# Kernel tuning notes

Measured on AMD Instinct MI355X. Metric: run time of the kernel, lower is better.

The kernel has to match this reference:

```python
import jax, jax.numpy as jnp
import numpy as np

LENS = 4.0
SCALE = 0.25
NUM_HEADS = 16


def _multispike(u):
    # floor(clamp(u, 0, 4) + 0.5)
    return jnp.floor(jnp.clip(u, 0.0, 4.0) + 0.5)


def _ms_act(x):
    # Multispike module: spike(4*x) / 4
    return _multispike(4.0 * x) / 4.0


def setup_inputs() -> dict:
    key = jax.random.key(0)
    ks = jax.random.split(key, 5)
    N, D = 65536, 1024
    x = jax.random.normal(ks[0], (N, D), dtype=jnp.float32)
    s = 1.0 / np.sqrt(D)
    Wq = jax.random.normal(ks[1], (D, D), dtype=jnp.float32) * s
    Wk = jax.random.normal(ks[2], (D, D), dtype=jnp.float32) * s
    Wv = jax.random.normal(ks[3], (D, D), dtype=jnp.float32) * s
    Wp = jax.random.normal(ks[4], (D, D), dtype=jnp.float32) * s
    return {"x": x, "Wq": Wq, "Wk": Wk, "Wv": Wv, "Wp": Wp}


def reference(x, Wq, Wk, Wv, Wp):
    N, C = x.shape
    H = NUM_HEADS
    hd = C // H

    xs = _ms_act(x)
    q = _ms_act(xs @ Wq.T)  # [N, C]
    k = _ms_act(xs @ Wk.T)
    v = _ms_act(xs @ Wv.T)

    q = q.reshape(N, H, hd)
    k = k.reshape(N, H, hd)
    v = v.reshape(N, H, hd)

    # linear attention: kv = k^T @ v per head -> [H, hd, hd]
    kv = jnp.einsum('nhd,nhe->hde', k, v)
    attn = jnp.einsum('nhd,hde->nhe', q, kv) * SCALE  # [N, H, hd]
    attn = attn.reshape(N, C)
    return attn @ Wp.T
```

## Files before the change

kernel.cpp:

```cpp
#include <hip/hip_runtime.h>
#include <hip/hip_bf16.h>


#define N_ROWS 65536
#define DIM    1024

using bf16x8 = __attribute__((ext_vector_type(8))) __bf16;
using f32x4  = __attribute__((ext_vector_type(4))) float;

__device__ __forceinline__ float ms_act(float u) {
    float t = fminf(fmaxf(4.0f * u, 0.0f), 4.0f);
    return floorf(t + 0.5f) * 0.25f;
}

__device__ __forceinline__ void gload_lds16(const void* g, void* l) {
    __builtin_amdgcn_global_load_lds(
        (__attribute__((address_space(1))) void*)g,
        (__attribute__((address_space(3))) void*)l, 16, 0, 0);
}

__global__ __launch_bounds__(256) void k0_convert_w(
    const float* __restrict__ Wq, const float* __restrict__ Wk,
    const float* __restrict__ Wv, __hip_bfloat16* __restrict__ Wb)
{
    const size_t M = (size_t)1024 * 1024;
    int b = blockIdx.x;
    int mat = b >> 10;
    const float* src = (mat == 0) ? Wq : ((mat == 1) ? Wk : Wv);
    size_t off = (size_t)(b & 1023) * 1024 + (size_t)threadIdx.x * 4;
    float4 u = *(const float4*)(src + off);
    const float* up = (const float*)&u;
    if (mat == 0) {
        union { __hip_bfloat16 h4[4]; uint2 u2; } hi, mid, lo;
#pragma unroll
        for (int i = 0; i < 4; ++i) {
            __hip_bfloat16 h = __float2bfloat16(up[i]);
            float r1 = up[i] - __bfloat162float(h);
            __hip_bfloat16 m = __float2bfloat16(r1);
            float r2 = r1 - __bfloat162float(m);
            hi.h4[i] = h; mid.h4[i] = m; lo.h4[i] = __float2bfloat16(r2);
        }
        *(uint2*)(Wb + 0 * M + off) = hi.u2;
        *(uint2*)(Wb + 3 * M + off) = mid.u2;
        *(uint2*)(Wb + 4 * M + off) = lo.u2;
    } else {
        union { __hip_bfloat16 h4[4]; uint2 u2; } o;
#pragma unroll
        for (int i = 0; i < 4; ++i) o.h4[i] = __float2bfloat16(up[i]);
        *(uint2*)(Wb + (size_t)mat * M + off) = o.u2;
    }
}

__global__ __launch_bounds__(256) void k0_quant_x(
    const float* __restrict__ x, __hip_bfloat16* __restrict__ xs)
{
    size_t i = ((size_t)blockIdx.x * 256 + threadIdx.x) * 4;
    float4 u = *(const float4*)(x + i);
    union { __hip_bfloat16 h4[4]; uint2 u2; } o;
    o.h4[0] = __float2bfloat16(ms_act(u.x)); o.h4[1] = __float2bfloat16(ms_act(u.y));
    o.h4[2] = __float2bfloat16(ms_act(u.z)); o.h4[3] = __float2bfloat16(ms_act(u.w));
    *(uint2*)(xs + i) = o.u2;
}

template <bool ACT>
__global__ __launch_bounds__(256) void gemm128(
    const __hip_bfloat16* __restrict__ A,
    const __hip_bfloat16* __restrict__ Bt,
    __hip_bfloat16* __restrict__ bout,
    float* __restrict__ fout,
    int npass, int off1, int off2)
{
    __shared__ __align__(16) __hip_bfloat16 lA[128 * 64];
    __shared__ __align__(16) __hip_bfloat16 lB[128 * 64];

    const int tid  = threadIdx.x;
    const int cb   = blockIdx.x, rb = blockIdx.y;
    const int wave = tid >> 6, lane = tid & 63;
    const int wm = wave >> 1, wn = wave & 1;
    const int lm = lane & 15, kg = lane >> 4;

    const int row0 = rb * 128, col0 = cb * 128;
    const int srow = tid >> 3;
    const int scol = (tid & 7) * 8;

    f32x4 acc[4][4] = {};

    const __hip_bfloat16* ag = A + (size_t)(row0 + srow) * DIM + scol;
    __hip_bfloat16* la = &lA[srow * 64 + scol];
    __hip_bfloat16* lb = &lB[srow * 64 + scol];

    const int np = ACT ? ((cb < 8) ? npass : 1) : npass;

    for (int p = 0; p < np; ++p) {
        const int cbase = (p == 0) ? col0
                        : ((p == 1) ? off1 + (col0 & 1023)
                                    : off2 + (col0 & 1023));
        const __hip_bfloat16* bg = Bt + (size_t)(cbase + srow) * DIM + scol;

        for (int k0 = 0; k0 < DIM; k0 += 64) {
#pragma unroll
            for (int q = 0; q < 4; ++q) {
                gload_lds16(ag + (size_t)q * 32 * DIM + k0, la + q * 32 * 64);
                gload_lds16(bg + (size_t)q * 32 * DIM + k0, lb + q * 32 * 64);
            }
            __syncthreads();
#pragma unroll
            for (int ks = 0; ks < 2; ++ks) {
                bf16x8 af[4], bfr[4];
#pragma unroll
                for (int i = 0; i < 4; ++i)
                    af[i] = *(const bf16x8*)&lA[(wm * 64 + i * 16 + lm) * 64 + ks * 32 + kg * 8];
#pragma unroll
                for (int j = 0; j < 4; ++j)
                    bfr[j] = *(const bf16x8*)&lB[(wn * 64 + j * 16 + lm) * 64 + ks * 32 + kg * 8];
#pragma unroll
                for (int i = 0; i < 4; ++i)
#pragma unroll
                    for (int j = 0; j < 4; ++j)
                        acc[i][j] = __builtin_amdgcn_mfma_f32_16x16x32_bf16(
                            af[i], bfr[j], acc[i][j], 0, 0, 0);
            }
            __syncthreads();
        }
    }

    const int r0 = row0 + wm * 64;
    if (ACT) {
        const int mi = cb >> 3;
        __hip_bfloat16* dst = bout + (size_t)mi * ((size_t)N_ROWS * DIM);
        const int c0 = (col0 & 1023) + wn * 64;
#pragma unroll
        for (int i = 0; i < 4; ++i)
#pragma unroll
            for (int j = 0; j < 4; ++j)
#pragma unroll
                for (int r = 0; r < 4; ++r) {
                    int row = r0 + i * 16 + kg * 4 + r;
                    int col = c0 + j * 16 + lm;
                    dst[(size_t)row * DIM + col] = __float2bfloat16(ms_act(acc[i][j][r]));
                }
    } else {
        const int c0 = col0 + wn * 64;
#pragma unroll
        for (int i = 0; i < 4; ++i)
#pragma unroll
            for (int j = 0; j < 4; ++j)
#pragma unroll
                for (int r = 0; r < 4; ++r) {
                    int row = r0 + i * 16 + kg * 4 + r;
                    int col = c0 + j * 16 + lm;
                    fout[(size_t)row * DIM + col] = acc[i][j][r];
                }
    }
}

__global__ __launch_bounds__(256) void k3_kv(
    const __hip_bfloat16* __restrict__ kb, const __hip_bfloat16* __restrict__ vb,
    float* __restrict__ kv)
{
    const int h = blockIdx.y;
    const int chunk = blockIdx.x;
    const int tid = threadIdx.x;
    __shared__ float lk[64][64];
    __shared__ float lv[64][64];
    float acc[4][4] = {};
    const int d0 = (tid & 15) * 4, e0 = (tid >> 4) * 4;
    const int r = tid >> 3, c8 = (tid & 7) * 8;

    for (int s = 0; s < 16; ++s) {
        const size_t n0 = (size_t)chunk * 1024 + (size_t)s * 64;
        __syncthreads();
#pragma unroll
        for (int p = 0; p < 2; ++p) {
            int row = p * 32 + r;
            uint4 kd = *(const uint4*)(kb + (n0 + row) * DIM + h * 64 + c8);
            uint4 vd = *(const uint4*)(vb + (n0 + row) * DIM + h * 64 + c8);
            float* dk = &lk[row][c8];
            float* dv = &lv[row][c8];
            dk[0] = __uint_as_float(kd.x << 16); dk[1] = __uint_as_float(kd.x & 0xffff0000u);
            dk[2] = __uint_as_float(kd.y << 16); dk[3] = __uint_as_float(kd.y & 0xffff0000u);
            dk[4] = __uint_as_float(kd.z << 16); dk[5] = __uint_as_float(kd.z & 0xffff0000u);
            dk[6] = __uint_as_float(kd.w << 16); dk[7] = __uint_as_float(kd.w & 0xffff0000u);
            dv[0] = __uint_as_float(vd.x << 16); dv[1] = __uint_as_float(vd.x & 0xffff0000u);
            dv[2] = __uint_as_float(vd.y << 16); dv[3] = __uint_as_float(vd.y & 0xffff0000u);
            dv[4] = __uint_as_float(vd.z << 16); dv[5] = __uint_as_float(vd.z & 0xffff0000u);
            dv[6] = __uint_as_float(vd.w << 16); dv[7] = __uint_as_float(vd.w & 0xffff0000u);
        }
        __syncthreads();
#pragma unroll 4
        for (int n = 0; n < 64; ++n) {
            float4 kk = *(const float4*)&lk[n][d0];
            float4 vv = *(const float4*)&lv[n][e0];
            const float* kp = (const float*)&kk;
#pragma unroll
            for (int i = 0; i < 4; ++i) {
                acc[i][0] = fmaf(kp[i], vv.x, acc[i][0]);
                acc[i][1] = fmaf(kp[i], vv.y, acc[i][1]);
                acc[i][2] = fmaf(kp[i], vv.z, acc[i][2]);
                acc[i][3] = fmaf(kp[i], vv.w, acc[i][3]);
            }
        }
    }
#pragma unroll
    for (int i = 0; i < 4; ++i)
#pragma unroll
        for (int j = 0; j < 4; ++j)
            atomicAdd(&kv[(h * 64 + d0 + i) * 64 + e0 + j], acc[i][j]);
}

__global__ __launch_bounds__(256) void k4_build_M(
    const float* __restrict__ kv, const float* __restrict__ Wp,
    __hip_bfloat16* __restrict__ Mt)
{
    const int j = blockIdx.x;
    const int c0 = threadIdx.x * 4;
    const int hh = c0 >> 6;
    const int d0 = c0 & 63;
    float s[4] = {0, 0, 0, 0};
    const float* kvh = kv + (size_t)hh * 64 * 64;
    const float* wp  = Wp + (size_t)j * DIM + hh * 64;
    for (int e = 0; e < 64; e += 4) {
        float4 w = *(const float4*)(wp + e);
#pragma unroll
        for (int i = 0; i < 4; ++i) {
            float4 a = *(const float4*)(kvh + (d0 + i) * 64 + e);
            s[i] += a.x * w.x + a.y * w.y + a.z * w.z + a.w * w.w;
        }
    }
    union { __hip_bfloat16 h4[4]; uint2 u2; } hi, lo;
#pragma unroll
    for (int i = 0; i < 4; ++i) {
        float m = 0.25f * s[i];
        __hip_bfloat16 h = __float2bfloat16(m);
        hi.h4[i] = h;
        lo.h4[i] = __float2bfloat16(m - __bfloat162float(h));
    }
    *(uint2*)(Mt + (size_t)j * DIM + c0) = hi.u2;
    *(uint2*)(Mt + (size_t)(1024 + j) * DIM + c0) = lo.u2;
}

extern "C" void kernel_launch(void* const* d_in, const int* in_sizes, int n_in,
                              void* d_out, int out_size, void* d_ws, size_t ws_size,
                              hipStream_t stream) {
    const float* x  = (const float*)d_in[0];
    const float* Wq = (const float*)d_in[1];
    const float* Wk = (const float*)d_in[2];
    const float* Wv = (const float*)d_in[3];
    const float* Wp = (const float*)d_in[4];
    float* out = (float*)d_out;

    char* ws = (char*)d_ws;
    const size_t MB = 1024ull * 1024;
    __hip_bfloat16* xs  = (__hip_bfloat16*)(ws);
    __hip_bfloat16* qkv = (__hip_bfloat16*)(ws + 128 * MB);
    __hip_bfloat16* Wb  = (__hip_bfloat16*)(ws + 512 * MB);
    __hip_bfloat16* Mt  = (__hip_bfloat16*)(ws + 522 * MB);
    float*          kv  = (float*)(ws + 526 * MB);

    k0_convert_w<<<3072, 256, 0, stream>>>(Wq, Wk, Wv, Wb);
    k0_quant_x<<<65536, 256, 0, stream>>>(x, xs);
    hipMemsetAsync(kv, 0, 16 * 64 * 64 * sizeof(float), stream);

    gemm128<true><<<dim3(24, 512), 256, 0, stream>>>(
        xs, Wb, qkv, nullptr, 3, 3072, 4096);

    k3_kv<<<dim3(64, 16), 256, 0, stream>>>(
        qkv + 1ull * N_ROWS * DIM, qkv + 2ull * N_ROWS * DIM, kv);

    k4_build_M<<<1024, 256, 0, stream>>>(kv, Wp, Mt);

    gemm128<false><<<dim3(8, 512), 256, 0, stream>>>(
        qkv, Mt, nullptr, out, 2, 1024, 0);
}
```

Measured before the change: 1.708 ms.

## Replace 128x128 GEMM with 256x256 multi-stage pipelined GEMM using swizzled LDS

After: 1.500 ms. 1.14x faster.

```diff
diff --git a/kernel.cpp b/kernel.cpp
--- a/kernel.cpp
+++ b/kernel.cpp
@@ -63,74 +63,124 @@
 }
 
 template <bool ACT>
-__global__ __launch_bounds__(256) void gemm128(
+__global__ __launch_bounds__(512, 2) void gemm256(
     const __hip_bfloat16* __restrict__ A,
     const __hip_bfloat16* __restrict__ Bt,
     __hip_bfloat16* __restrict__ bout,
     float* __restrict__ fout,
     int npass, int off1, int off2)
 {
-    __shared__ __align__(16) __hip_bfloat16 lA[128 * 64];
-    __shared__ __align__(16) __hip_bfloat16 lB[128 * 64];
+    __shared__ __align__(1024) char lds[131072];
 
     const int tid  = threadIdx.x;
-    const int cb   = blockIdx.x, rb = blockIdx.y;
-    const int wave = tid >> 6, lane = tid & 63;
-    const int wm = wave >> 1, wn = wave & 1;
+    const int lane = tid & 63;
+    const int wave = tid >> 6;
     const int lm = lane & 15, kg = lane >> 4;
-
-    const int row0 = rb * 128, col0 = cb * 128;
-    const int srow = tid >> 3;
-    const int scol = (tid & 7) * 8;
-
-    f32x4 acc[4][4] = {};
-
-    const __hip_bfloat16* ag = A + (size_t)(row0 + srow) * DIM + scol;
-    __hip_bfloat16* la = &lA[srow * 64 + scol];
-    __hip_bfloat16* lb = &lB[srow * 64 + scol];
-
-    const int np = ACT ? ((cb < 8) ? npass : 1) : npass;
-
-    for (int p = 0; p < np; ++p) {
-        const int cbase = (p == 0) ? col0
-                        : ((p == 1) ? off1 + (col0 & 1023)
-                                    : off2 + (col0 & 1023));
-        const __hip_bfloat16* bg = Bt + (size_t)(cbase + srow) * DIM + scol;
-
-        for (int k0 = 0; k0 < DIM; k0 += 64) {
-#pragma unroll
-            for (int q = 0; q < 4; ++q) {
-                gload_lds16(ag + (size_t)q * 32 * DIM + k0, la + q * 32 * 64);
-                gload_lds16(bg + (size_t)q * 32 * DIM + k0, lb + q * 32 * 64);
-            }
-            __syncthreads();
-#pragma unroll
-            for (int ks = 0; ks < 2; ++ks) {
-                bf16x8 af[4], bfr[4];
-#pragma unroll
-                for (int i = 0; i < 4; ++i)
-                    af[i] = *(const bf16x8*)&lA[(wm * 64 + i * 16 + lm) * 64 + ks * 32 + kg * 8];
-#pragma unroll
-                for (int j = 0; j < 4; ++j)
-                    bfr[j] = *(const bf16x8*)&lB[(wn * 64 + j * 16 + lm) * 64 + ks * 32 + kg * 8];
-#pragma unroll
-                for (int i = 0; i < 4; ++i)
-#pragma unroll
-                    for (int j = 0; j < 4; ++j)
-                        acc[i][j] = __builtin_amdgcn_mfma_f32_16x16x32_bf16(
-                            af[i], bfr[j], acc[i][j], 0, 0, 0);
-            }
-            __syncthreads();
-        }
-    }
-
-    const int r0 = row0 + wm * 64;
+    const int wm = wave >> 2, wn = wave & 3;
+
+    const int cb = blockIdx.x, rb = blockIdx.y;
+    const int row0 = rb * 256, col0 = cb * 256;
+    const int np = ACT ? ((cb < 4) ? npass : 1) : npass;
+    const int CMAX = np * 64;
+
+    const int gsw   = (kg ^ ((lm >> 1) & 3)) * 16;
+    const int aBase = (wm * 128 + lm) * 64 + gsw;
+    const int bBase = (wn * 64 + lm) * 64 + gsw;
+
+    const int I0 = tid, I1 = 512 + tid;
+    const int r0g = I0 >> 2, r1g = I1 >> 2;
+    const int g0 = (I0 & 3) ^ ((r0g >> 1) & 3);
+    const int g1 = (I1 & 3) ^ ((r1g >> 1) & 3);
+    const size_t aoff0 = (size_t)r0g * DIM + g0 * 8;
+    const size_t aoff1 = (size_t)r1g * DIM + g1 * 8;
+    const int ldso0 = I0 * 16, ldso1 = I1 * 16;
+    const __hip_bfloat16* Arow = A + (size_t)row0 * DIM;
+
+    f32x4 acc[8][4] = {};
+
+    auto stage = [&](int cc) {
+        const int h = cc >> 1, slot = h & 3, tile = h >> 1;
+        const int k0 = ((tile & 15) << 6) + ((h & 1) << 5);
+        if (cc & 1) {
+            char* d = lds + slot * 16384;
+            gload_lds16(Arow + aoff0 + k0, d + ldso0);
+            gload_lds16(Arow + aoff1 + k0, d + ldso1);
+        } else {
+            const int pass = tile >> 4;
+            const int cbase = (pass == 0) ? col0
+                            : ((pass == 1) ? off1 + (col0 & 1023)
+                                           : off2 + (col0 & 1023));
+            const __hip_bfloat16* Brow = Bt + (size_t)cbase * DIM;
+            char* d = lds + 65536 + slot * 16384;
+            gload_lds16(Brow + aoff0 + k0, d + ldso0);
+            gload_lds16(Brow + aoff1 + k0, d + ldso1);
+        }
+    };
+
+    int c = 0;
+#pragma unroll
+    for (int i = 0; i < 7; ++i) { stage(c); ++c; }
+    asm volatile("s_waitcnt vmcnt(6)" ::: "memory");
+    __builtin_amdgcn_s_barrier();
+
+    bf16x8 af[4], bfr[4];
+
+#define LD_B(S) do {                                                         \
+    const char* bp_ = lds + 65536 + (S) * 16384 + bBase;                     \
+    bfr[0] = *(const bf16x8*)(bp_);                                          \
+    bfr[1] = *(const bf16x8*)(bp_ + 1024);                                   \
+    bfr[2] = *(const bf16x8*)(bp_ + 2048);                                   \
+    bfr[3] = *(const bf16x8*)(bp_ + 3072);                                   \
+} while (0)
+
+#define LD_A(S, MH) do {                                                     \
+    const char* ap_ = lds + (S) * 16384 + aBase + (MH) * 4096;               \
+    af[0] = *(const bf16x8*)(ap_);                                           \
+    af[1] = *(const bf16x8*)(ap_ + 1024);                                    \
+    af[2] = *(const bf16x8*)(ap_ + 2048);                                    \
+    af[3] = *(const bf16x8*)(ap_ + 3072);                                    \
+} while (0)
+
+#define PHASE(S, MH, BND) do {                                               \
+    if ((MH) == 0) LD_B(S);                                                  \
+    LD_A(S, MH);                                                             \
+    if (c < CMAX) stage(c);                                                  \
+    ++c;                                                                     \
+    __builtin_amdgcn_s_barrier();                                            \
+    asm volatile("s_waitcnt lgkmcnt(0)" ::: "memory");                       \
+    __builtin_amdgcn_sched_barrier(0);                                       \
+    __builtin_amdgcn_s_setprio(1);                                           \
+    _Pragma("unroll")                                                        \
+    for (int i2_ = 0; i2_ < 4; ++i2_) {                                      \
+        _Pragma("unroll")                                                    \
+        for (int j_ = 0; j_ < 4; ++j_)                                       \
+            acc[(MH) * 4 + i2_][j_] = __builtin_amdgcn_mfma_f32_16x16x32_bf16( \
+                af[i2_], bfr[j_], acc[(MH) * 4 + i2_][j_], 0, 0, 0);         \
+    }                                                                        \
+    __builtin_amdgcn_s_setprio(0);                                           \
+    __builtin_amdgcn_sched_barrier(0);                                       \
+    if (BND) asm volatile("s_waitcnt vmcnt(6)" ::: "memory");                \
+    __builtin_amdgcn_s_barrier();                                            \
+} while (0)
+
+    for (int it = 0; it < np * 8; ++it) {
+        PHASE(0, 0, false); PHASE(0, 1, false);
+        PHASE(1, 0, false); PHASE(1, 1, true);
+        PHASE(2, 0, false); PHASE(2, 1, false);
+        PHASE(3, 0, false); PHASE(3, 1, true);
+    }
+
+#undef PHASE
+#undef LD_A
+#undef LD_B
+
+    const int r0 = row0 + wm * 128;
     if (ACT) {
-        const int mi = cb >> 3;
+        const int mi = cb >> 2;
         __hip_bfloat16* dst = bout + (size_t)mi * ((size_t)N_ROWS * DIM);
         const int c0 = (col0 & 1023) + wn * 64;
 #pragma unroll
-        for (int i = 0; i < 4; ++i)
+        for (int i = 0; i < 8; ++i)
 #pragma unroll
             for (int j = 0; j < 4; ++j)
 #pragma unroll
@@ -142,7 +192,7 @@
     } else {
         const int c0 = col0 + wn * 64;
 #pragma unroll
-        for (int i = 0; i < 4; ++i)
+        for (int i = 0; i < 8; ++i)
 #pragma unroll
             for (int j = 0; j < 4; ++j)
 #pragma unroll
@@ -261,7 +311,7 @@
     k0_quant_x<<<65536, 256, 0, stream>>>(x, xs);
     hipMemsetAsync(kv, 0, 16 * 64 * 64 * sizeof(float), stream);
 
-    gemm128<true><<<dim3(24, 512), 256, 0, stream>>>(
+    gemm256<true><<<dim3(12, 256), 512, 0, stream>>>(
         xs, Wb, qkv, nullptr, 3, 3072, 4096);
 
     k3_kv<<<dim3(64, 16), 256, 0, stream>>>(
@@ -269,6 +319,6 @@
 
     k4_build_M<<<1024, 256, 0, stream>>>(kv, Wp, Mt);
 
-    gemm128<false><<<dim3(8, 512), 256, 0, stream>>>(
+    gemm256<false><<<dim3(4, 256), 512, 0, stream>>>(
         qkv, Mt, nullptr, out, 2, 1024, 0);
 }
```
